# Kernel optimization log

Measured on AMD Instinct MI355X. Metric: run time of the kernel, lower is better.

Reference implementation:

```python
import jax, jax.numpy as jnp
import numpy as np

N_NODES = 50000
N_EDGES = 400000
HEADS = 3
CH = 128
NEG_SLOPE = 0.2
EPS = 1e-16


def setup_inputs() -> dict:
    key = jax.random.key(0)
    ks = jax.random.split(key, 10)
    return {
        "x": jax.random.normal(ks[0], (N_NODES, 9), jnp.float32),
        "emb_w": jax.random.normal(ks[1], (9, 128), jnp.float32) * 0.1,
        "emb_b": jax.random.normal(ks[2], (128,), jnp.float32) * 0.1,
        "gat_w": jax.random.normal(ks[3], (128, HEADS * CH), jnp.float32) * 0.05,
        "att_src": jax.random.normal(ks[4], (HEADS, CH), jnp.float32) * 0.1,
        "att_dst": jax.random.normal(ks[5], (HEADS, CH), jnp.float32) * 0.1,
        "gat_bias": jax.random.normal(ks[6], (CH,), jnp.float32) * 0.1,
        "out_w": jax.random.normal(ks[7], (128, 4), jnp.float32) * 0.1,
        "out_b": jax.random.normal(ks[8], (4,), jnp.float32) * 0.1,
        "edge_index": jax.random.randint(ks[9], (2, N_EDGES), 0, N_NODES, jnp.int64 if jax.config.jax_enable_x64 else jnp.int32),
    }


def reference(x, emb_w, emb_b, gat_w, att_src, att_dst, gat_bias, out_w, out_b, edge_index):
    n = x.shape[0]
    h = x @ emb_w + emb_b                                   # [N,128]
    # add self loops (PyG GATConv default)
    loops = jnp.arange(n, dtype=edge_index.dtype)
    src = jnp.concatenate([edge_index[0], loops])
    dst = jnp.concatenate([edge_index[1], loops])
    xh = (h @ gat_w).reshape(n, HEADS, CH)                  # [N,H,C]
    a_src = jnp.einsum('nhc,hc->nh', xh, att_src)           # [N,H]
    a_dst = jnp.einsum('nhc,hc->nh', xh, att_dst)           # [N,H]
    e = a_src[src] + a_dst[dst]                             # [E,H]
    e = jax.nn.leaky_relu(e, NEG_SLOPE)
    # segment softmax over destination node
    e_max = jax.ops.segment_max(e, dst, num_segments=n)
    e = jnp.exp(e - e_max[dst])
    denom = jax.ops.segment_sum(e, dst, num_segments=n)
    alpha = e / (denom[dst] + EPS)                          # [E,H]
    msg = xh[src] * alpha[:, :, None]                       # [E,H,C]
    agg = jax.ops.segment_sum(msg, dst, num_segments=n)     # [N,H,C]
    out = agg.mean(axis=1) + gat_bias                       # concat=False -> head mean
    x_new = out + h                                         # residual
    return x_new @ out_w + out_b                            # [N,4]
```

## Files before the change

### kernel.cpp

```cpp
#include <hip/hip_runtime.h>
#include <hip/hip_bf16.h>
#include <cstdint>

#define NEG 0.2f
#define SBS 256

typedef __attribute__((ext_vector_type(8))) short bf16x8;
typedef __attribute__((ext_vector_type(8))) unsigned short ushort8;
typedef __attribute__((ext_vector_type(4))) float f32x4;

__device__ __forceinline__ float bf2f(unsigned short u){
  return __uint_as_float(((unsigned)u)<<16);
}
__device__ __forceinline__ unsigned short f2bf(float f){
  __hip_bfloat16 b = __float2bfloat16(f);
  return *reinterpret_cast<unsigned short*>(&b);
}

__global__ __launch_bounds__(256)
void embed_kernel(const float* __restrict__ x, const float* __restrict__ emb_w,
                  const float* __restrict__ emb_b, const float* __restrict__ gat_w,
                  const float* __restrict__ att_src, const float* __restrict__ att_dst,
                  unsigned short* __restrict__ h_bf, float* __restrict__ a_s,
                  float* __restrict__ a_d, int* __restrict__ deg,
                  int* __restrict__ gcount, int nN)
{
  __shared__ float watt[768];
  int tid = threadIdx.x;

  #pragma unroll
  for (int r=0;r<3;r++){
    int o = tid + r*256;
    int isD = (o >= 384);
    int t2 = isD ? (o-384) : o;
    int h = t2 >> 7, k = t2 & 127;
    const float* att = isD ? (att_dst + h*128) : (att_src + h*128);
    const float* gw  = gat_w + (size_t)k*384 + h*128;
    float dot = 0.f;
    #pragma unroll 8
    for (int c=0;c<128;c++) dot += gw[c]*att[c];
    watt[o] = dot;
  }
  __syncthreads();

  int n = blockIdx.x*256 + tid;
  if (n < nN) deg[n] = 0;
  if (blockIdx.x==0 && tid==0) gcount[0] = 0;
  if (n >= nN) return;

  float xv[9];
  #pragma unroll
  for (int k=0;k<9;k++) xv[k] = x[(size_t)n*9 + k];

  float s0=0.f,s1=0.f,s2=0.f, d0=0.f,d1=0.f,d2=0.f;
  unsigned short* hrow = h_bf + (size_t)n*128;

  #pragma unroll 4
  for (int c0=0; c0<128; c0+=8){
    unsigned short pk[8];
    #pragma unroll
    for (int j=0;j<8;j++){
      int c = c0 + j;
      float acc = emb_b[c];
      #pragma unroll
      for (int k=0;k<9;k++) acc += xv[k]*emb_w[k*128+c];
      pk[j] = f2bf(acc);
      s0 += acc*watt[c]; s1 += acc*watt[128+c]; s2 += acc*watt[256+c];
      d0 += acc*watt[384+c]; d1 += acc*watt[512+c]; d2 += acc*watt[640+c];
    }
    *(int4*)(hrow + c0) = *(int4*)pk;
  }
  a_s[(size_t)n*3+0]=s0; a_s[(size_t)n*3+1]=s1; a_s[(size_t)n*3+2]=s2;
  a_d[(size_t)n*3+0]=d0; a_d[(size_t)n*3+1]=d1; a_d[(size_t)n*3+2]=d2;
}

__global__ __launch_bounds__(256)
void deg_kernel(const int* __restrict__ ei, int* __restrict__ deg,
                const float* __restrict__ gat_w,
                unsigned short* __restrict__ Bt2, int nE, int ebN)
{
  if (blockIdx.x < (unsigned)ebN){
    int e = blockIdx.x*256 + threadIdx.x;
    if (e < nE) atomicAdd(&deg[ei[nE + e]], 1);
  } else {
    int i = (blockIdx.x - ebN)*256 + threadIdx.x;
    if (i < 12*128*32){
      int ks  = i >> 12;
      int rem = i & 4095;
      int col = rem >> 5;
      int kk  = rem & 31;
      int t = ks*32 + kk;
      int h = t >> 7, k = t & 127;
      Bt2[i] = f2bf(gat_w[(size_t)k*384 + h*128 + col] * (1.f/3.f));
    }
  }
}

__global__ __launch_bounds__(256)
void alloc_kernel(const int* __restrict__ deg, int* __restrict__ gcount,
                  int* __restrict__ rowptr, int* __restrict__ cursor, int nN)
{
  int tid = threadIdx.x, wave = tid>>6, lane = tid&63;
  int n = blockIdx.x*256 + tid;
  int v = (n < nN) ? deg[n]+1 : 0;
  int sc = v;
  #pragma unroll
  for (int off=1; off<64; off<<=1){
    int t = __shfl_up(sc, off);
    if (lane >= off) sc += t;
  }
  __shared__ int ws[4];
  __shared__ int bbase;
  if (lane==63) ws[wave] = sc;
  __syncthreads();
  if (tid==0) bbase = atomicAdd(gcount, ws[0]+ws[1]+ws[2]+ws[3]);
  __syncthreads();
  int wbase = 0;
  for (int i=0;i<wave;i++) wbase += ws[i];
  int excl = bbase + wbase + sc - v;
  if (n < nN){ rowptr[n] = excl; cursor[n] = excl; }
}

__global__ __launch_bounds__(256)
void scatter_kernel(const int* __restrict__ ei, int* __restrict__ cursor,
                    const float* __restrict__ a_s, const float* __restrict__ a_d,
                    const int* __restrict__ rowptr, const int* __restrict__ deg,
                    float4* __restrict__ val, int nE, int ebN, int nN)
{
  if (blockIdx.x < (unsigned)ebN){
    int e = blockIdx.x*256 + threadIdx.x;
    if (e < nE){
      int s = ei[e], d = ei[nE + e];
      float e0 = a_s[(size_t)s*3+0] + a_d[(size_t)d*3+0]; e0 = e0>0.f ? e0 : NEG*e0;
      float e1 = a_s[(size_t)s*3+1] + a_d[(size_t)d*3+1]; e1 = e1>0.f ? e1 : NEG*e1;
      float e2 = a_s[(size_t)s*3+2] + a_d[(size_t)d*3+2]; e2 = e2>0.f ? e2 : NEG*e2;
      int pos = atomicAdd(&cursor[d], 1);
      val[pos] = make_float4(__expf(e0), __expf(e1), __expf(e2), __int_as_float(s));
    }
  } else {
    int n = (blockIdx.x - ebN)*256 + threadIdx.x;
    if (n < nN){
      float e0 = a_s[(size_t)n*3+0] + a_d[(size_t)n*3+0]; e0 = e0>0.f ? e0 : NEG*e0;
      float e1 = a_s[(size_t)n*3+1] + a_d[(size_t)n*3+1]; e1 = e1>0.f ? e1 : NEG*e1;
      float e2 = a_s[(size_t)n*3+2] + a_d[(size_t)n*3+2]; e2 = e2>0.f ? e2 : NEG*e2;
      val[rowptr[n] + deg[n]] = make_float4(__expf(e0), __expf(e1), __expf(e2),
                                            __int_as_float(n));
    }
  }
}

__global__ __launch_bounds__(256)
void gathermm_kernel(const int* __restrict__ rowptr, const int* __restrict__ deg,
                     const float4* __restrict__ val,
                     const unsigned short* __restrict__ h_bf,
                     const unsigned short* __restrict__ Bt2,
                     const float* __restrict__ gat_bias,
                     const float* __restrict__ out_w, const float* __restrict__ out_b,
                     float* __restrict__ out, int nN)
{
  __shared__ __align__(16) unsigned short hs[32][392];
  int tid = threadIdx.x;
  int wave = tid >> 6, lane = tid & 63;
  int g = lane >> 4, lin = lane & 15;
  int nb0 = blockIdx.x*32;

  for (int pass=0; pass<2; ++pass){
    int local = pass*16 + wave*4 + g;
    int n = nb0 + local;
    int valid = (n < nN);
    int nc = valid ? n : 0;
    int ro   = rowptr[nc];
    int degT = valid ? (deg[nc] + 1) : 0;

    float a0[8], a1[8], a2[8];
    #pragma unroll
    for (int c=0;c<8;c++){ a0[c]=0.f; a1[c]=0.f; a2[c]=0.f; }
    float den0=0.f, den1=0.f, den2=0.f;

    const unsigned short* hb = h_bf + 8*lin;
    const float4* vrow = val + ro;

    int j = 0;
    for (; j+1 < degT; j += 2){
      float4 vA = vrow[j];
      float4 vB = vrow[j+1];
      int sA = __float_as_int(vA.w);
      int sB = __float_as_int(vB.w);
      ushort8 ha = *(const ushort8*)(hb + (size_t)sA*128);
      ushort8 hc = *(const ushort8*)(hb + (size_t)sB*128);
      den0 += vA.x + vB.x; den1 += vA.y + vB.y; den2 += vA.z + vB.z;
      #pragma unroll
      for (int c=0;c<8;c++){
        float fa = bf2f(ha[c]), fb = bf2f(hc[c]);
        a0[c] += vA.x*fa + vB.x*fb;
        a1[c] += vA.y*fa + vB.y*fb;
        a2[c] += vA.z*fa + vB.z*fb;
      }
    }
    if (j < degT){
      float4 vA = vrow[j];
      int sA = __float_as_int(vA.w);
      ushort8 ha = *(const ushort8*)(hb + (size_t)sA*128);
      den0 += vA.x; den1 += vA.y; den2 += vA.z;
      #pragma unroll
      for (int c=0;c<8;c++){
        float fa = bf2f(ha[c]);
        a0[c] += vA.x*fa; a1[c] += vA.y*fa; a2[c] += vA.z*fa;
      }
    }

    if (valid){
      float w0 = 1.f/(den0+1e-16f);
      float w1 = 1.f/(den1+1e-16f);
      float w2 = 1.f/(den2+1e-16f);
      unsigned short o0[8], o1[8], o2[8];
      #pragma unroll
      for (int c=0;c<8;c++){
        o0[c] = f2bf(a0[c]*w0);
        o1[c] = f2bf(a1[c]*w1);
        o2[c] = f2bf(a2[c]*w2);
      }
      unsigned short* hp = &hs[local][8*lin];
      *(int4*)(hp      ) = *(int4*)o0;
      *(int4*)(hp + 128) = *(int4*)o1;
      *(int4*)(hp + 256) = *(int4*)o2;
    }
  }
  __syncthreads();

  if (wave >= 2) return;
  int cl = lane & 15, kg = lane >> 4;
  int rlocal = wave*16 + cl;
  const unsigned short* aBase = &hs[rlocal][0];

  f32x4 acc[8];
  #pragma unroll
  for (int f=0;f<8;f++) acc[f] = (f32x4){0.f,0.f,0.f,0.f};

  #pragma unroll
  for (int ks=0; ks<12; ks++){
    bf16x8 a = *(const bf16x8*)(aBase + ks*32 + kg*8);
    #pragma unroll
    for (int f=0;f<8;f++){
      bf16x8 b = *(const bf16x8*)(Bt2 + (size_t)ks*4096 + (f*16 + cl)*32 + kg*8);
      acc[f] = __builtin_amdgcn_mfma_f32_16x16x32_bf16(a, b, acc[f], 0, 0, 0);
    }
  }

  float p[4][4];
  #pragma unroll
  for (int r=0;r<4;r++)
    #pragma unroll
    for (int j2=0;j2<4;j2++) p[r][j2]=0.f;

  int r0 = nb0 + wave*16;
  #pragma unroll
  for (int f=0;f<8;f++){
    int col = f*16 + cl;
    float bias = gat_bias[col];
    float w0=out_w[col*4+0], w1=out_w[col*4+1], w2=out_w[col*4+2], w3=out_w[col*4+3];
    #pragma unroll
    for (int r=0;r<4;r++){
      int row = r0 + kg*4 + r;
      float hres = (row < nN) ? bf2f(h_bf[(size_t)row*128 + col]) : 0.f;
      float xn = acc[f][r] + bias + hres;
      p[r][0] += xn*w0; p[r][1] += xn*w1; p[r][2] += xn*w2; p[r][3] += xn*w3;
    }
  }
  #pragma unroll
  for (int off=1; off<16; off<<=1){
    #pragma unroll
    for (int r=0;r<4;r++)
      #pragma unroll
      for (int j2=0;j2<4;j2++) p[r][j2] += __shfl_xor(p[r][j2], off);
  }
  if (cl == 0){
    #pragma unroll
    for (int r=0;r<4;r++){
      int row = r0 + kg*4 + r;
      if (row < nN){
        float4 o = {p[r][0]+out_b[0], p[r][1]+out_b[1], p[r][2]+out_b[2], p[r][3]+out_b[3]};
        *(float4*)(out + (size_t)row*4) = o;
      }
    }
  }
}

extern "C" void kernel_launch(void* const* d_in, const int* in_sizes, int n_in,
                              void* d_out, int out_size, void* d_ws, size_t ws_size,
                              hipStream_t stream) {
  const float* x       = (const float*)d_in[0];
  const float* emb_w   = (const float*)d_in[1];
  const float* emb_b   = (const float*)d_in[2];
  const float* gat_w   = (const float*)d_in[3];
  const float* att_src = (const float*)d_in[4];
  const float* att_dst = (const float*)d_in[5];
  const float* gat_bias= (const float*)d_in[6];
  const float* out_w   = (const float*)d_in[7];
  const float* out_b   = (const float*)d_in[8];
  const int*   ei      = (const int*)d_in[9];
  float* out = (float*)d_out;

  int nN = in_sizes[0]/9;
  int nE = in_sizes[9]/2;
  int nB = (nN + SBS - 1) / SBS;
  int ebN = (nE + 255)/256;

  char* p = (char*)d_ws;
  auto alloc = [&](size_t bytes)->char*{
    char* r = p; p += (bytes + 255) & ~(size_t)255; return r;
  };
  unsigned short* h_bf   = (unsigned short*)alloc((size_t)nN*128*2);
  float*          a_s    = (float*)         alloc((size_t)nN*3*4);
  float*          a_d    = (float*)         alloc((size_t)nN*3*4);
  unsigned short* Bt2    = (unsigned short*)alloc((size_t)12*128*32*2);
  int*            deg    = (int*)           alloc((size_t)nN*4);
  int*            rowptr = (int*)           alloc((size_t)nN*4);
  int*            cursor = (int*)           alloc((size_t)nN*4);
  int*            gcount = (int*)           alloc(256);
  float4*         val    = (float4*)        alloc(((size_t)nE+nN)*16);

  embed_kernel<<<nB, 256, 0, stream>>>(
      x, emb_w, emb_b, gat_w, att_src, att_dst, h_bf, a_s, a_d, deg, gcount, nN);

  deg_kernel<<<ebN + 192, 256, 0, stream>>>(ei, deg, gat_w, Bt2, nE, ebN);

  alloc_kernel<<<nB, 256, 0, stream>>>(deg, gcount, rowptr, cursor, nN);

  scatter_kernel<<<ebN + nB, 256, 0, stream>>>(
      ei, cursor, a_s, a_d, rowptr, deg, val, nE, ebN, nN);

  gathermm_kernel<<<(nN+31)/32, 256, 0, stream>>>(
      rowptr, deg, val, h_bf, Bt2, gat_bias, out_w, out_b, out, nN);
}
```

Baseline: 212.8 us.

## Split fused gather+MFMA kernel into gather and LDS-staged double-buffered GEMM kernels

Splits the fused gather-then-matmul kernel in two. A gather kernel writes the attention-weighted aggregated features (bf16, 384 per node) to a global buffer. A separate GEMM kernel then stages the weight matrix into padded LDS with double buffering, so all four waves compute MFMAs instead of two. This removes the idle half-block during the matmul phase and the repeated global reads of B, but adds a write and read of a roughly 38MB intermediate plus an extra launch.

After: 206.2 us. 3.1% less time.

```diff
diff --git a/kernel.cpp b/kernel.cpp
--- a/kernel.cpp
+++ b/kernel.cpp
@@ -4,6 +4,7 @@
 
 #define NEG 0.2f
 #define SBS 256
+#define PADK 56
 
 typedef __attribute__((ext_vector_type(8))) short bf16x8;
 typedef __attribute__((ext_vector_type(8))) unsigned short ushort8;
@@ -150,110 +151,136 @@
 }
 
 __global__ __launch_bounds__(256)
-void gathermm_kernel(const int* __restrict__ rowptr, const int* __restrict__ deg,
-                     const float4* __restrict__ val,
-                     const unsigned short* __restrict__ h_bf,
-                     const unsigned short* __restrict__ Bt2,
-                     const float* __restrict__ gat_bias,
-                     const float* __restrict__ out_w, const float* __restrict__ out_b,
-                     float* __restrict__ out, int nN)
-{
-  __shared__ __align__(16) unsigned short hs[32][392];
-  int tid = threadIdx.x;
+void gather_kernel(const int* __restrict__ rowptr, const int* __restrict__ deg,
+                   const float4* __restrict__ val,
+                   const unsigned short* __restrict__ h_bf,
+                   unsigned short* __restrict__ hagg, int nN)
+{
+  int wave = threadIdx.x >> 6, lane = threadIdx.x & 63;
+  int g   = lane >> 4;
+  int lin = lane & 15;
+  int n = blockIdx.x*16 + wave*4 + g;
+  int valid = (n < nN);
+  int nc = valid ? n : (nN-1);
+
+  int ro   = rowptr[nc];
+  int degT = valid ? (deg[nc] + 1) : 0;
+
+  float a0[8], a1[8], a2[8];
+  #pragma unroll
+  for (int c=0;c<8;c++){ a0[c]=0.f; a1[c]=0.f; a2[c]=0.f; }
+  float den0=0.f, den1=0.f, den2=0.f;
+
+  const unsigned short* hb = h_bf + 8*lin;
+  const float4* vrow = val + ro;
+
+  int j = 0;
+  for (; j+1 < degT; j += 2){
+    float4 vA = vrow[j];
+    float4 vB = vrow[j+1];
+    int sA = __float_as_int(vA.w);
+    int sB = __float_as_int(vB.w);
+    ushort8 ha = *(const ushort8*)(hb + (size_t)sA*128);
+    ushort8 hc = *(const ushort8*)(hb + (size_t)sB*128);
+    den0 += vA.x + vB.x; den1 += vA.y + vB.y; den2 += vA.z + vB.z;
+    #pragma unroll
+    for (int c=0;c<8;c++){
+      float fa = bf2f(ha[c]), fb = bf2f(hc[c]);
+      a0[c] += vA.x*fa + vB.x*fb;
+      a1[c] += vA.y*fa + vB.y*fb;
+      a2[c] += vA.z*fa + vB.z*fb;
+    }
+  }
+  if (j < degT){
+    float4 vA = vrow[j];
+    int sA = __float_as_int(vA.w);
+    ushort8 ha = *(const ushort8*)(hb + (size_t)sA*128);
+    den0 += vA.x; den1 += vA.y; den2 += vA.z;
+    #pragma unroll
+    for (int c=0;c<8;c++){
+      float fa = bf2f(ha[c]);
+      a0[c] += vA.x*fa; a1[c] += vA.y*fa; a2[c] += vA.z*fa;
+    }
+  }
+
+  if (valid){
+    float w0 = 1.f/(den0+1e-16f);
+    float w1 = 1.f/(den1+1e-16f);
+    float w2 = 1.f/(den2+1e-16f);
+    unsigned short o0[8], o1[8], o2[8];
+    #pragma unroll
+    for (int c=0;c<8;c++){
+      o0[c] = f2bf(a0[c]*w0);
+      o1[c] = f2bf(a1[c]*w1);
+      o2[c] = f2bf(a2[c]*w2);
+    }
+    size_t bi = (size_t)n*384 + 8*lin;
+    *(int4*)(hagg + bi      ) = *(int4*)o0;
+    *(int4*)(hagg + bi + 128) = *(int4*)o1;
+    *(int4*)(hagg + bi + 256) = *(int4*)o2;
+  }
+}
+
+__global__ __launch_bounds__(256)
+void gemm2_kernel(const unsigned short* __restrict__ hagg,
+                  const unsigned short* __restrict__ Bt2,
+                  const unsigned short* __restrict__ h_bf,
+                  const float* __restrict__ gat_bias,
+                  const float* __restrict__ out_w, const float* __restrict__ out_b,
+                  float* __restrict__ out, int nN)
+{
+  __shared__ __align__(16) unsigned short Bs[2][128*PADK];
+  int tid  = threadIdx.x;
   int wave = tid >> 6, lane = tid & 63;
-  int g = lane >> 4, lin = lane & 15;
-  int nb0 = blockIdx.x*32;
-
-  for (int pass=0; pass<2; ++pass){
-    int local = pass*16 + wave*4 + g;
-    int n = nb0 + local;
-    int valid = (n < nN);
-    int nc = valid ? n : 0;
-    int ro   = rowptr[nc];
-    int degT = valid ? (deg[nc] + 1) : 0;
-
-    float a0[8], a1[8], a2[8];
-    #pragma unroll
-    for (int c=0;c<8;c++){ a0[c]=0.f; a1[c]=0.f; a2[c]=0.f; }
-    float den0=0.f, den1=0.f, den2=0.f;
-
-    const unsigned short* hb = h_bf + 8*lin;
-    const float4* vrow = val + ro;
-
-    int j = 0;
-    for (; j+1 < degT; j += 2){
-      float4 vA = vrow[j];
-      float4 vB = vrow[j+1];
-      int sA = __float_as_int(vA.w);
-      int sB = __float_as_int(vB.w);
-      ushort8 ha = *(const ushort8*)(hb + (size_t)sA*128);
-      ushort8 hc = *(const ushort8*)(hb + (size_t)sB*128);
-      den0 += vA.x + vB.x; den1 += vA.y + vB.y; den2 += vA.z + vB.z;
-      #pragma unroll
-      for (int c=0;c<8;c++){
-        float fa = bf2f(ha[c]), fb = bf2f(hc[c]);
-        a0[c] += vA.x*fa + vB.x*fb;
-        a1[c] += vA.y*fa + vB.y*fb;
-        a2[c] += vA.z*fa + vB.z*fb;
-      }
-    }
-    if (j < degT){
-      float4 vA = vrow[j];
-      int sA = __float_as_int(vA.w);
-      ushort8 ha = *(const ushort8*)(hb + (size_t)sA*128);
-      den0 += vA.x; den1 += vA.y; den2 += vA.z;
-      #pragma unroll
-      for (int c=0;c<8;c++){
-        float fa = bf2f(ha[c]);
-        a0[c] += vA.x*fa; a1[c] += vA.y*fa; a2[c] += vA.z*fa;
-      }
-    }
-
-    if (valid){
-      float w0 = 1.f/(den0+1e-16f);
-      float w1 = 1.f/(den1+1e-16f);
-      float w2 = 1.f/(den2+1e-16f);
-      unsigned short o0[8], o1[8], o2[8];
-      #pragma unroll
-      for (int c=0;c<8;c++){
-        o0[c] = f2bf(a0[c]*w0);
-        o1[c] = f2bf(a1[c]*w1);
-        o2[c] = f2bf(a2[c]*w2);
-      }
-      unsigned short* hp = &hs[local][8*lin];
-      *(int4*)(hp      ) = *(int4*)o0;
-      *(int4*)(hp + 128) = *(int4*)o1;
-      *(int4*)(hp + 256) = *(int4*)o2;
-    }
-  }
+  int cl = lane & 15, kg = lane >> 4;
+  int r0 = blockIdx.x*64 + wave*16;
+  int rowA = min(r0 + cl, nN-1);
+  const unsigned short* aBase = hagg + (size_t)rowA*384 + kg*8;
+
+  int scol = tid >> 1, shalf = tid & 1;
+  int dstI = scol*(PADK/8) + shalf*2;
+
+  {
+    const int4* src = (const int4*)Bt2;
+    int4 t0 = src[2*tid], t1 = src[2*tid+1];
+    ((int4*)Bs[0])[dstI]   = t0;
+    ((int4*)Bs[0])[dstI+1] = t1;
+  }
+  f32x4 acc[8];
+  #pragma unroll
+  for (int f=0;f<8;f++) acc[f] = (f32x4){0.f,0.f,0.f,0.f};
+  bf16x8 aCur = *(const bf16x8*)(aBase);
   __syncthreads();
 
-  if (wave >= 2) return;
-  int cl = lane & 15, kg = lane >> 4;
-  int rlocal = wave*16 + cl;
-  const unsigned short* aBase = &hs[rlocal][0];
-
-  f32x4 acc[8];
-  #pragma unroll
-  for (int f=0;f<8;f++) acc[f] = (f32x4){0.f,0.f,0.f,0.f};
-
   #pragma unroll
   for (int ks=0; ks<12; ks++){
-    bf16x8 a = *(const bf16x8*)(aBase + ks*32 + kg*8);
+    int4 t0, t1; bf16x8 aNext;
+    if (ks < 11){
+      const int4* src = (const int4*)(Bt2 + (size_t)(ks+1)*4096);
+      t0 = src[2*tid]; t1 = src[2*tid+1];
+      aNext = *(const bf16x8*)(aBase + (ks+1)*32);
+    }
+    const unsigned short* bs = Bs[ks & 1];
     #pragma unroll
     for (int f=0;f<8;f++){
-      bf16x8 b = *(const bf16x8*)(Bt2 + (size_t)ks*4096 + (f*16 + cl)*32 + kg*8);
-      acc[f] = __builtin_amdgcn_mfma_f32_16x16x32_bf16(a, b, acc[f], 0, 0, 0);
-    }
+      bf16x8 b = *(const bf16x8*)(bs + (f*16 + cl)*PADK + kg*8);
+      acc[f] = __builtin_amdgcn_mfma_f32_16x16x32_bf16(aCur, b, acc[f], 0, 0, 0);
+    }
+    if (ks < 11){
+      int4* dst = (int4*)Bs[(ks+1) & 1];
+      dst[dstI]   = t0;
+      dst[dstI+1] = t1;
+      aCur = aNext;
+    }
+    __syncthreads();
   }
 
   float p[4][4];
   #pragma unroll
   for (int r=0;r<4;r++)
     #pragma unroll
-    for (int j2=0;j2<4;j2++) p[r][j2]=0.f;
-
-  int r0 = nb0 + wave*16;
+    for (int j=0;j<4;j++) p[r][j]=0.f;
+
   #pragma unroll
   for (int f=0;f<8;f++){
     int col = f*16 + cl;
@@ -272,7 +299,7 @@
     #pragma unroll
     for (int r=0;r<4;r++)
       #pragma unroll
-      for (int j2=0;j2<4;j2++) p[r][j2] += __shfl_xor(p[r][j2], off);
+      for (int j=0;j<4;j++) p[r][j] += __shfl_xor(p[r][j], off);
   }
   if (cl == 0){
     #pragma unroll
@@ -319,6 +346,7 @@
   int*            cursor = (int*)           alloc((size_t)nN*4);
   int*            gcount = (int*)           alloc(256);
   float4*         val    = (float4*)        alloc(((size_t)nE+nN)*16);
+  unsigned short* hagg   = (unsigned short*)alloc((size_t)nN*384*2);
 
   embed_kernel<<<nB, 256, 0, stream>>>(
       x, emb_w, emb_b, gat_w, att_src, att_dst, h_bf, a_s, a_d, deg, gcount, nN);
@@ -330,6 +358,9 @@
   scatter_kernel<<<ebN + nB, 256, 0, stream>>>(
       ei, cursor, a_s, a_d, rowptr, deg, val, nE, ebN, nN);
 
-  gathermm_kernel<<<(nN+31)/32, 256, 0, stream>>>(
-      rowptr, deg, val, h_bf, Bt2, gat_bias, out_w, out_b, out, nN);
-}
+  gather_kernel<<<(nN+15)/16, 256, 0, stream>>>(
+      rowptr, deg, val, h_bf, hagg, nN);
+
+  gemm2_kernel<<<(nN+63)/64, 256, 0, stream>>>(
+      hagg, Bt2, h_bf, gat_bias, out_w, out_b, out, nN);
+}
```
